# Kernel tuning notes

Hardware: AMD Instinct MI355X
Metric: run time of the kernel (lower is better)

The kernel has to match this reference:

```python
import jax, jax.numpy as jnp
import numpy as np

D_MODEL = 1024
NUM_HEADS = 16
HEAD_DIM = D_MODEL // NUM_HEADS  # 64
SEQ = 2048
BATCH = 4
LN_EPS = 1e-5


def setup_inputs() -> dict:
    key = jax.random.key(0)
    k_in, k_qkv, k_o, k_g = jax.random.split(key, 4)
    inputs = jax.random.normal(k_in, (BATCH, SEQ, D_MODEL), dtype=jnp.float32)
    mask = jnp.zeros((BATCH, 1, SEQ, SEQ), dtype=jnp.float32)  # additive mask
    # Realistic rotary embeddings (RoPE), duplicated-halves layout
    inv_freq = 1.0 / (10000.0 ** (jnp.arange(0, HEAD_DIM, 2, dtype=jnp.float32) / HEAD_DIM))
    pos = jnp.arange(SEQ, dtype=jnp.float32)
    freqs = pos[:, None] * inv_freq[None, :]            # [S, Dh/2]
    emb = jnp.concatenate([freqs, freqs], axis=-1)       # [S, Dh]
    cos = jnp.cos(emb)
    sin = jnp.sin(emb)
    # Parameters
    sd = 1.0 / np.sqrt(D_MODEL)
    w_qkv = jax.random.normal(k_qkv, (D_MODEL, 3 * D_MODEL), dtype=jnp.float32) * sd
    w_o = jax.random.normal(k_o, (D_MODEL, D_MODEL), dtype=jnp.float32) * sd
    ln_gamma = jnp.ones((D_MODEL,), dtype=jnp.float32)
    return {"inputs": inputs, "mask": mask, "cos": cos, "sin": sin,
            "ln_gamma": ln_gamma, "w_qkv": w_qkv, "w_o": w_o}


def _rotate_half(x):
    x1, x2 = jnp.split(x, 2, axis=-1)
    return jnp.concatenate([-x2, x1], axis=-1)


def reference(inputs, mask, cos, sin, ln_gamma, w_qkv, w_o):
    B, S, D = inputs.shape
    # Pre-attention LayerNorm (layer_id != 0), center=False -> no beta
    mu = jnp.mean(inputs, axis=-1, keepdims=True)
    var = jnp.mean(jnp.square(inputs - mu), axis=-1, keepdims=True)
    x = (inputs - mu) / jnp.sqrt(var + LN_EPS) * ln_gamma
    # Fused QKV projection, split into heads: [B, H, S, Dh]
    qkv = (x @ w_qkv).reshape(B, S, 3, NUM_HEADS, HEAD_DIM)
    qkv = jnp.transpose(qkv, (2, 0, 3, 1, 4))
    q, k, v = qkv[0], qkv[1], qkv[2]
    # RoPE
    c = cos.reshape(1, 1, S, HEAD_DIM)
    s = sin.reshape(1, 1, S, HEAD_DIM)
    q = q * c + _rotate_half(q) * s
    k = k * c + _rotate_half(k) * s
    # Scaled dot-product attention with additive mask
    scale = 1.0 / jnp.sqrt(jnp.asarray(HEAD_DIM, dtype=q.dtype))
    logits = jnp.einsum("bhqd,bhkd->bhqk", q, k) * scale + mask
    attn = jax.nn.softmax(logits, axis=-1)
    out = jnp.einsum("bhqk,bhkd->bhqd", attn, v)
    out = jnp.transpose(out, (0, 2, 1, 3)).reshape(B, S, D)
    return out @ w_o
```

## Files before the change

kernel.cpp:

```cpp
#include <hip/hip_runtime.h>
#include <stdint.h>

#define DEV __device__ __forceinline__

typedef __bf16 bf16x8 __attribute__((ext_vector_type(8)));
typedef float f32x4 __attribute__((ext_vector_type(4)));
typedef float f32x16 __attribute__((ext_vector_type(16)));

DEV unsigned short f2bf(float f) {
  union { float f; uint32_t u; } c; c.f = f;
  uint32_t u = c.u;
  u += 0x7FFFu + ((u >> 16) & 1u);
  return (unsigned short)(u >> 16);
}
DEV float bf2f(unsigned short h) {
  union { uint32_t u; float f; } c; c.u = ((uint32_t)h) << 16;
  return c.f;
}
DEV float u2f(uint32_t u) {
  union { uint32_t u; float f; } c; c.u = u;
  return c.f;
}
DEV bf16x8 ld8(const unsigned short* p) {
  uint4 u = *reinterpret_cast<const uint4*>(p);
  return __builtin_bit_cast(bf16x8, u);
}
DEV uint32_t cvtpk(float lo, float hi) {
  uint32_t r;
  asm("v_cvt_pk_bf16_f32 %0, %1, %2" : "=v"(r) : "v"(lo), "v"(hi));
  return r;
}
DEV void permswap(uint32_t& a, uint32_t& b) {
  asm("v_permlane32_swap_b32 %0, %1" : "+v"(a), "+v"(b));
}
DEV float exp2b(float x) { return __builtin_amdgcn_exp2f(x); }
DEV void gload16(const void* g, void* l) {
  __builtin_amdgcn_global_load_lds((const __attribute__((address_space(1))) void*)g,
                                   (__attribute__((address_space(3))) void*)l, 16, 0, 0);
}

template<int K, int N>
__global__ __launch_bounds__(256)
void transpose_cast_kernel(const float* __restrict__ in, unsigned short* __restrict__ out) {
  __shared__ float tile[64][65];
  const int bk = blockIdx.x % (K / 64);
  const int bn = blockIdx.x / (K / 64);
  const int k0 = bk * 64, n0 = bn * 64;
  const int t = threadIdx.x;
#pragma unroll
  for (int i = 0; i < 16; ++i) {
    int idx = t + i * 256;
    int kl = idx >> 6, nl = idx & 63;
    tile[kl][nl] = in[(size_t)(k0 + kl) * N + n0 + nl];
  }
  __syncthreads();
#pragma unroll
  for (int i = 0; i < 16; ++i) {
    int idx = t + i * 256;
    int nl = idx >> 6, kl = idx & 63;
    out[(size_t)(n0 + nl) * K + k0 + kl] = f2bf(tile[kl][nl]);
  }
}

__global__ __launch_bounds__(256)
void ln_kernel(const float* __restrict__ x, const float* __restrict__ gamma,
               unsigned short* __restrict__ y) {
  const int row = blockIdx.x;
  const int t = threadIdx.x;
  const float4 v = reinterpret_cast<const float4*>(x + (size_t)row * 1024)[t];
  float s  = v.x + v.y + v.z + v.w;
  float s2 = v.x * v.x + v.y * v.y + v.z * v.z + v.w * v.w;
#pragma unroll
  for (int off = 1; off < 64; off <<= 1) {
    s  += __shfl_xor(s, off);
    s2 += __shfl_xor(s2, off);
  }
  __shared__ float red[8];
  const int w = t >> 6, lane = t & 63;
  if (lane == 0) { red[w] = s; red[4 + w] = s2; }
  __syncthreads();
  s  = red[0] + red[1] + red[2] + red[3];
  s2 = red[4] + red[5] + red[6] + red[7];
  const float mu = s * (1.0f / 1024.0f);
  const float var = s2 * (1.0f / 1024.0f) - mu * mu;
  const float rstd = rsqrtf(var + 1e-5f);
  const float4 g = reinterpret_cast<const float4*>(gamma)[t];
  ushort4 o;
  o.x = f2bf((v.x - mu) * rstd * g.x);
  o.y = f2bf((v.y - mu) * rstd * g.y);
  o.z = f2bf((v.z - mu) * rstd * g.z);
  o.w = f2bf((v.w - mu) * rstd * g.w);
  reinterpret_cast<ushort4*>(y + (size_t)row * 1024)[t] = o;
}

template<int N_DIM, bool OUT_F32>
__global__ __launch_bounds__(256)
void gemm_bt_kernel(const unsigned short* __restrict__ A,
                    const unsigned short* __restrict__ Bt,
                    void* __restrict__ Cout) {
  constexpr int K = 1024;
  __shared__ unsigned short a_lds[128 * 32];
  __shared__ unsigned short b_lds[128 * 32];
  const int t = threadIdx.x;
  const int w = t >> 6, l = t & 63;
  const int lrow = l & 15, lch = l >> 4;
  const int nbn = N_DIM / 128;
  const int m0 = (blockIdx.x / nbn) * 128;
  const int n0 = (blockIdx.x % nbn) * 128;
  const int wm = (w >> 1) * 64, wn = (w & 1) * 64;

  const int srow = t >> 2;
  const int schk = t & 3;
  const int scol = ((schk ^ (srow & 3)) << 3);
  const unsigned short* aS0 = A  + (size_t)(m0 + srow) * K + scol;
  const unsigned short* aS1 = A  + (size_t)(m0 + 64 + srow) * K + scol;
  const unsigned short* bS0 = Bt + (size_t)(n0 + srow) * K + scol;
  const unsigned short* bS1 = Bt + (size_t)(n0 + 64 + srow) * K + scol;
  unsigned short* aD0 = a_lds + (w * 16) * 32;
  unsigned short* aD1 = a_lds + (64 + w * 16) * 32;
  unsigned short* bD0 = b_lds + (w * 16) * 32;
  unsigned short* bD1 = b_lds + (64 + w * 16) * 32;

  f32x4 acc[4][4] = {};

  for (int k0 = 0; k0 < K; k0 += 32) {
    gload16(aS0 + k0, aD0);
    gload16(aS1 + k0, aD1);
    gload16(bS0 + k0, bD0);
    gload16(bS1 + k0, bD1);
    __syncthreads();
    bf16x8 af[4], bfr[4];
#pragma unroll
    for (int m = 0; m < 4; ++m) {
      int row = wm + m * 16 + lrow;
      af[m] = ld8(a_lds + row * 32 + ((lch ^ (lrow & 3)) << 3));
    }
#pragma unroll
    for (int n = 0; n < 4; ++n) {
      int row = wn + n * 16 + lrow;
      bfr[n] = ld8(b_lds + row * 32 + ((lch ^ (lrow & 3)) << 3));
    }
#pragma unroll
    for (int m = 0; m < 4; ++m)
#pragma unroll
      for (int n = 0; n < 4; ++n)
        acc[m][n] = __builtin_amdgcn_mfma_f32_16x16x32_bf16(af[m], bfr[n], acc[m][n], 0, 0, 0);
    __syncthreads();
  }

#pragma unroll
  for (int m = 0; m < 4; ++m) {
    const int grow0 = m0 + wm + m * 16 + lch * 4;
#pragma unroll
    for (int n = 0; n < 4; ++n) {
      const int gcol = n0 + wn + n * 16 + lrow;
#pragma unroll
      for (int r = 0; r < 4; ++r) {
        if constexpr (OUT_F32)
          ((float*)Cout)[(size_t)(grow0 + r) * N_DIM + gcol] = acc[m][n][r];
        else
          ((unsigned short*)Cout)[(size_t)(grow0 + r) * N_DIM + gcol] = f2bf(acc[m][n][r]);
      }
    }
  }
}

__global__ __launch_bounds__(256)
void rope_split_kernel(const unsigned short* __restrict__ qkv,
                       const float* __restrict__ cosb,
                       const float* __restrict__ sinb,
                       unsigned short* __restrict__ Qo,
                       unsigned short* __restrict__ Ko,
                       unsigned short* __restrict__ Vo) {
  const int bid = blockIdx.x;
  const int sb = bid & 31, h = (bid >> 5) & 15, b = bid >> 9;
  const int s0 = sb * 64;
  const int t = threadIdx.x;
  __shared__ unsigned short qt[64][72], kt[64][72], vt[64][72];

  const int sl = t >> 2, c0 = (t & 3) * 16;
  {
    const size_t base = (size_t)(b * 2048 + s0 + sl) * 3072 + h * 64 + c0;
    uint4 q1 = *(const uint4*)(qkv + base);
    uint4 q2 = *(const uint4*)(qkv + base + 8);
    uint4 k1 = *(const uint4*)(qkv + base + 1024);
    uint4 k2 = *(const uint4*)(qkv + base + 1032);
    uint4 v1 = *(const uint4*)(qkv + base + 2048);
    uint4 v2 = *(const uint4*)(qkv + base + 2056);
    *(uint4*)&qt[sl][c0] = q1; *(uint4*)&qt[sl][c0 + 8] = q2;
    *(uint4*)&kt[sl][c0] = k1; *(uint4*)&kt[sl][c0 + 8] = k2;
    *(uint4*)&vt[sl][c0] = v1; *(uint4*)&vt[sl][c0 + 8] = v2;
  }
  __syncthreads();
  {
    const int sg = s0 + sl;
    alignas(16) unsigned short qo16[16], ko16[16];
#pragma unroll
    for (int j = 0; j < 16; ++j) {
      const int d = c0 + j;
      const float cv = cosb[sg * 64 + d], sv = sinb[sg * 64 + d];
      const float qv = bf2f(qt[sl][d]), qp = bf2f(qt[sl][d ^ 32]);
      const float kv = bf2f(kt[sl][d]), kp = bf2f(kt[sl][d ^ 32]);
      const float rq = qv * cv + ((d < 32) ? -qp : qp) * sv;
      const float rk = kv * cv + ((d < 32) ? -kp : kp) * sv;
      qo16[j] = f2bf(rq * 0.180336880f);
      ko16[j] = f2bf(rk);
    }
    const size_t ob = ((size_t)(b * 16 + h) * 2048 + sg) * 64 + c0;
    *(uint4*)(Qo + ob) = *(uint4*)qo16; *(uint4*)(Qo + ob + 8) = *(uint4*)(qo16 + 8);
    *(uint4*)(Ko + ob) = *(uint4*)ko16; *(uint4*)(Ko + ob + 8) = *(uint4*)(ko16 + 8);
  }
  {
    const int dh = t >> 2, sc0 = (t & 3) * 16;
    alignas(16) unsigned short vo16[16];
#pragma unroll
    for (int j = 0; j < 16; ++j) vo16[j] = vt[sc0 + j][dh];
    const size_t ob = ((size_t)(b * 16 + h) * 64 + dh) * 2048 + s0 + sc0;
    *(uint4*)(Vo + ob) = *(uint4*)vo16; *(uint4*)(Vo + ob + 8) = *(uint4*)(vo16 + 8);
  }
}

__global__ __launch_bounds__(256)
void mask_prep_kernel(const float* __restrict__ mask, unsigned short* __restrict__ mrs,
                      unsigned char* __restrict__ flg) {
  const int bid = blockIdx.x;
  const int kvt = bid & 31, qc = (bid >> 5) & 31, b = bid >> 10;
  const int t = threadIdx.x;
  __shared__ float tile[64][72];
  __shared__ int nzf;
  if (t == 0) nzf = 0;
  uint32_t orbits = 0;
  {
    const int r = t >> 2, c0 = (t & 3) * 16;
    const float* src = mask + (size_t)b * (2048ull * 2048) + (size_t)(qc * 64 + r) * 2048 + kvt * 64 + c0;
#pragma unroll
    for (int i = 0; i < 4; ++i) {
      const float4 v = *(const float4*)(src + i * 4);
      *(float4*)&tile[r][c0 + i * 4] = v;
      orbits |= __float_as_uint(v.x) | __float_as_uint(v.y) |
                __float_as_uint(v.z) | __float_as_uint(v.w);
    }
  }
  __syncthreads();
  if (orbits != 0u) nzf = 1;
  __syncthreads();
  if (nzf) {
    const int cid = t >> 5;
    const int n = cid >> 2, jj = (cid >> 1) & 1, hi = cid & 1;
    const int qq0 = (t & 31) * 2;
    const int cb = n * 32 + jj * 16 + hi * 4;
    unsigned short* dst = mrs + (((size_t)(b * 32 + kvt) * 8 + cid) * 2048 + qc * 64) * 8;
#pragma unroll
    for (int qo = 0; qo < 2; ++qo) {
      const int q = qq0 + qo;
      alignas(16) unsigned short o8[8];
#pragma unroll
      for (int v = 0; v < 8; ++v) {
        const int col = cb + (v >> 2) * 8 + (v & 3);
        o8[v] = f2bf(tile[q][col] * 1.44269504f);
      }
      *(uint4*)(dst + (size_t)q * 8) = *(uint4*)o8;
    }
  }
  if (t == 0) flg[(size_t)(b * 32 + kvt) * 32 + qc] = (unsigned char)nzf;
}

__global__ __launch_bounds__(256)
void attn_kernel(const unsigned short* __restrict__ Q,
                 const unsigned short* __restrict__ Kg,
                 const unsigned short* __restrict__ Vt,
                 const unsigned short* __restrict__ mrs,
                 const unsigned char* __restrict__ flg,
                 unsigned short* __restrict__ O) {
  const int t = threadIdx.x, w = t >> 6, l = t & 63;
  const int lq = l & 31, hi = l >> 5;
  const int bid = blockIdx.x;
  const int x = bid & 7, y = bid >> 3;
  const int bh = x * 8 + (y & 7), qb = y >> 3;
  const int b = bh >> 4, h = bh & 15;
  const int q0 = qb * 128 + w * 32;

  const unsigned short* Qb = Q  + (size_t)bh * (2048 * 64);
  const unsigned short* Kb = Kg + (size_t)bh * (2048 * 64);
  const unsigned short* Vb = Vt + (size_t)bh * (64 * 2048);
  const unsigned short* ml = mrs + (size_t)b * 4194304 + (size_t)hi * 16384 + (size_t)(q0 + lq) * 8;
  const unsigned char* fb = flg + (size_t)(b * 32) * 32 + qb * 2;

  __shared__ unsigned short k_lds[2][64 * 64];
  __shared__ unsigned short v_lds[2][64 * 64];

  bf16x8 qf[4];
  {
    const unsigned short* qp = Qb + (size_t)(q0 + lq) * 64 + hi * 8;
#pragma unroll
    for (int c = 0; c < 4; ++c) qf[c] = ld8(qp + c * 16);
  }
  bf16x8 ones;
  {
    const uint4 ou = { 0x3F803F80u, 0x3F803F80u, 0x3F803F80u, 0x3F803F80u };
    ones = __builtin_bit_cast(bf16x8, ou);
  }

  const int srow = t >> 2, sl0 = (t & 3) * 2, sl1 = sl0 + 1;
  const unsigned short* ks = Kb + (size_t)srow * 64 + sl0 * 8;
  const unsigned short* vs = Vb + (size_t)srow * 2048 + sl0 * 8;
  const int wd0 = srow * 64 + ((sl0 ^ (srow & 7)) << 3);
  const int wd1 = srow * 64 + ((sl1 ^ (srow & 7)) << 3);

  uint4 ka0 = *(const uint4*)ks;
  uint4 ka1 = *(const uint4*)(ks + 8);
  uint4 va0 = *(const uint4*)vs;
  uint4 va1 = *(const uint4*)(vs + 8);
  *(uint4*)(k_lds[0] + wd0) = ka0;
  *(uint4*)(k_lds[0] + wd1) = ka1;
  *(uint4*)(v_lds[0] + wd0) = va0;
  *(uint4*)(v_lds[0] + wd1) = va1;

  f32x16 ot0 = {}, ot1 = {};
  f32x16 st_sum = {};
  int cur = 0;
  const int lsw = lq & 7;

  uint4 mA[4], mB[4];

  auto do_tile = [&](int kv0, uint4 (&mcur)[4], uint4 (&mnext)[4],
                     bool hm, bool hmn) {
    __syncthreads();
    const bool more = (kv0 + 64) < 2048;
    if (more) {
      ka0 = *(const uint4*)(ks + (size_t)(kv0 + 64) * 64);
      ka1 = *(const uint4*)(ks + (size_t)(kv0 + 64) * 64 + 8);
      va0 = *(const uint4*)(vs + kv0 + 64);
      va1 = *(const uint4*)(vs + kv0 + 64 + 8);
      if (hmn) {
        const unsigned short* mp = ml + (size_t)(kv0 + 64) * 2048;
#pragma unroll
        for (int c2 = 0; c2 < 4; ++c2) mnext[c2] = *(const uint4*)(mp + c2 * 32768);
      }
    }

    f32x16 st0 = {}, st1 = {};
    if (hm) {
#pragma unroll
      for (int jj = 0; jj < 2; ++jj) {
        const uint4 u0 = mcur[jj];
        const uint4 u1 = mcur[2 + jj];
#pragma unroll
        for (int wv = 0; wv < 4; ++wv) {
          const uint32_t w0 = ((const uint32_t*)&u0)[wv];
          const uint32_t w1 = ((const uint32_t*)&u1)[wv];
          st0[jj * 8 + wv * 2]     = u2f(w0 << 16);
          st0[jj * 8 + wv * 2 + 1] = u2f(w0 & 0xffff0000u);
          st1[jj * 8 + wv * 2]     = u2f(w1 << 16);
          st1[jj * 8 + wv * 2 + 1] = u2f(w1 & 0xffff0000u);
        }
      }
    }

    const unsigned short* kb = k_lds[cur];
    __builtin_amdgcn_s_setprio(1);
#pragma unroll
    for (int c = 0; c < 4; ++c) {
      const int so = (((2 * c + hi) ^ lsw) << 3);
      const bf16x8 kf0 = ld8(kb + lq * 64 + so);
      const bf16x8 kf1 = ld8(kb + (32 + lq) * 64 + so);
      st0 = __builtin_amdgcn_mfma_f32_32x32x16_bf16(kf0, qf[c], st0, 0, 0, 0);
      st1 = __builtin_amdgcn_mfma_f32_32x32x16_bf16(kf1, qf[c], st1, 0, 0, 0);
    }
    __builtin_amdgcn_s_setprio(0);

#pragma unroll
    for (int r = 0; r < 16; ++r) {
      st0[r] = exp2b(st0[r]);
      st1[r] = exp2b(st1[r]);
    }

    bf16x8 pa[4];
#pragma unroll
    for (int c = 0; c < 4; ++c) {
      const int e8 = (c & 1) * 8;
      uint32_t A01, B01, A23, B23;
      if (c < 2) {
        A01 = cvtpk(st0[e8 + 0], st0[e8 + 1]);
        B01 = cvtpk(st0[e8 + 4], st0[e8 + 5]);
        A23 = cvtpk(st0[e8 + 2], st0[e8 + 3]);
        B23 = cvtpk(st0[e8 + 6], st0[e8 + 7]);
      } else {
        A01 = cvtpk(st1[e8 + 0], st1[e8 + 1]);
        B01 = cvtpk(st1[e8 + 4], st1[e8 + 5]);
        A23 = cvtpk(st1[e8 + 2], st1[e8 + 3]);
        B23 = cvtpk(st1[e8 + 6], st1[e8 + 7]);
      }
      permswap(A01, B01);
      permswap(A23, B23);
      const uint4 pw = { A01, A23, B01, B23 };
      pa[c] = __builtin_bit_cast(bf16x8, pw);
    }

    if (more) {
      unsigned short* kn = k_lds[cur ^ 1];
      unsigned short* vn = v_lds[cur ^ 1];
      *(uint4*)(kn + wd0) = ka0;
      *(uint4*)(kn + wd1) = ka1;
      *(uint4*)(vn + wd0) = va0;
      *(uint4*)(vn + wd1) = va1;
    }

    const unsigned short* vb = v_lds[cur];
    __builtin_amdgcn_s_setprio(1);
#pragma unroll
    for (int c = 0; c < 4; ++c) {
      const int so = (((2 * c + hi) ^ lsw) << 3);
      const bf16x8 vf0 = ld8(vb + lq * 64 + so);
      const bf16x8 vf1 = ld8(vb + (32 + lq) * 64 + so);
      ot0 = __builtin_amdgcn_mfma_f32_32x32x16_bf16(vf0, pa[c], ot0, 0, 0, 0);
      ot1 = __builtin_amdgcn_mfma_f32_32x32x16_bf16(vf1, pa[c], ot1, 0, 0, 0);
      st_sum = __builtin_amdgcn_mfma_f32_32x32x16_bf16(ones, pa[c], st_sum, 0, 0, 0);
    }
    __builtin_amdgcn_s_setprio(0);
    cur ^= 1;
  };

  unsigned int bm = 0;
  for (int kvt = 0; kvt < 32; ++kvt) bm |= fb[kvt * 32] | fb[kvt * 32 + 1];

  if (bm == 0) {
    for (int kv0 = 0; kv0 < 2048; kv0 += 128) {
      do_tile(kv0, mA, mB, false, false);
      do_tile(kv0 + 64, mB, mA, false, false);
    }
  } else {
    bool hmA = (fb[0] | fb[1]) != 0;
    if (hmA) {
#pragma unroll
      for (int c2 = 0; c2 < 4; ++c2) mA[c2] = *(const uint4*)(ml + c2 * 32768);
    }
    bool hmB = false;
    for (int kv0 = 0; kv0 < 2048; kv0 += 128) {
      const int tB = (kv0 >> 6) + 1;
      hmB = (kv0 + 64 < 2048) && ((fb[tB * 32] | fb[tB * 32 + 1]) != 0);
      do_tile(kv0, mA, mB, hmA, hmB);
      const int tA = tB + 1;
      hmA = (kv0 + 128 < 2048) && ((fb[tA * 32] | fb[tA * 32 + 1]) != 0);
      do_tile(kv0 + 64, mB, mA, hmB, hmA);
    }
  }

  const float inv = 1.0f / st_sum[0];
  unsigned short* ob = O + ((size_t)(b * 2048 + q0 + lq) * 16 + h) * 64 + hi * 4;
#pragma unroll
  for (int td = 0; td < 2; ++td) {
#pragma unroll
    for (int rr = 0; rr < 4; ++rr) {
      ushort4 ov;
      if (td == 0) {
        ov.x = f2bf(ot0[rr * 4 + 0] * inv);
        ov.y = f2bf(ot0[rr * 4 + 1] * inv);
        ov.z = f2bf(ot0[rr * 4 + 2] * inv);
        ov.w = f2bf(ot0[rr * 4 + 3] * inv);
      } else {
        ov.x = f2bf(ot1[rr * 4 + 0] * inv);
        ov.y = f2bf(ot1[rr * 4 + 1] * inv);
        ov.z = f2bf(ot1[rr * 4 + 2] * inv);
        ov.w = f2bf(ot1[rr * 4 + 3] * inv);
      }
      *(ushort4*)(ob + td * 32 + rr * 8) = ov;
    }
  }
}

extern "C" void kernel_launch(void* const* d_in, const int* in_sizes, int n_in,
                              void* d_out, int out_size, void* d_ws, size_t ws_size,
                              hipStream_t stream) {
  (void)in_sizes; (void)n_in; (void)out_size; (void)ws_size;
  const float* x     = (const float*)d_in[0];
  const float* mask  = (const float*)d_in[1];
  const float* cosb  = (const float*)d_in[2];
  const float* sinb  = (const float*)d_in[3];
  const float* gamma = (const float*)d_in[4];
  const float* w_qkv = (const float*)d_in[5];
  const float* w_o   = (const float*)d_in[6];

  char* ws = (char*)d_ws;
  unsigned short* x_bf   = (unsigned short*)(ws);
  unsigned short* wqkvT  = (unsigned short*)(ws + 16777216);
  unsigned short* woT    = (unsigned short*)(ws + 23068672);
  unsigned short* qkv_bf = (unsigned short*)(ws + 25165824);
  unsigned short* q_r    = (unsigned short*)(ws + 75497472);
  unsigned short* k_r    = (unsigned short*)(ws + 92274688);
  unsigned short* v_t    = (unsigned short*)(ws + 109051904);
  unsigned short* attn   = (unsigned short*)(ws + 125829120);
  unsigned short* mask_rs = qkv_bf;
  unsigned char*  flags   = (unsigned char*)(ws + 25165824 + 33554432);

  transpose_cast_kernel<1024, 3072><<<dim3(16 * 48), dim3(256), 0, stream>>>(w_qkv, wqkvT);
  transpose_cast_kernel<1024, 1024><<<dim3(16 * 16), dim3(256), 0, stream>>>(w_o, woT);
  ln_kernel<<<dim3(8192), dim3(256), 0, stream>>>(x, gamma, x_bf);
  gemm_bt_kernel<3072, false><<<dim3(64 * 24), dim3(256), 0, stream>>>(x_bf, wqkvT, (void*)qkv_bf);
  rope_split_kernel<<<dim3(4 * 16 * 32), dim3(256), 0, stream>>>(qkv_bf, cosb, sinb, q_r, k_r, v_t);
  mask_prep_kernel<<<dim3(4096), dim3(256), 0, stream>>>(mask, mask_rs, flags);
  attn_kernel<<<dim3(1024), dim3(256), 0, stream>>>(q_r, k_r, v_t, mask_rs, flags, attn);
  gemm_bt_kernel<1024, true><<<dim3(64 * 8), dim3(256), 0, stream>>>(attn, woT, d_out);
}
```

Measured before the change: 237.4 us.

## Pre-swizzle K/V into MFMA fragment layout and load directly to registers

```diff
diff --git a/kernel.cpp b/kernel.cpp
--- a/kernel.cpp
+++ b/kernel.cpp
@@ -170,8 +170,8 @@
                        const float* __restrict__ cosb,
                        const float* __restrict__ sinb,
                        unsigned short* __restrict__ Qo,
-                       unsigned short* __restrict__ Ko,
-                       unsigned short* __restrict__ Vo) {
+                       unsigned short* __restrict__ Kf,
+                       unsigned short* __restrict__ Vf) {
   const int bid = blockIdx.x;
   const int sb = bid & 31, h = (bid >> 5) & 15, b = bid >> 9;
   const int s0 = sb * 64;
@@ -192,6 +192,7 @@
     *(uint4*)&vt[sl][c0] = v1; *(uint4*)&vt[sl][c0 + 8] = v2;
   }
   __syncthreads();
+  const size_t fbase = (size_t)(b * 16 + h) * 131072;
   {
     const int sg = s0 + sl;
     alignas(16) unsigned short qo16[16], ko16[16];
@@ -208,15 +209,18 @@
     }
     const size_t ob = ((size_t)(b * 16 + h) * 2048 + sg) * 64 + c0;
     *(uint4*)(Qo + ob) = *(uint4*)qo16; *(uint4*)(Qo + ob + 8) = *(uint4*)(qo16 + 8);
-    *(uint4*)(Ko + ob) = *(uint4*)ko16; *(uint4*)(Ko + ob + 8) = *(uint4*)(ko16 + 8);
+    unsigned short* kd = Kf + fbase + ((size_t)((sb * 2 + (sl >> 5)) * 4 + (t & 3))) * 512;
+    *(uint4*)(kd + (sl & 31) * 8)        = *(uint4*)ko16;
+    *(uint4*)(kd + (32 + (sl & 31)) * 8) = *(uint4*)(ko16 + 8);
   }
   {
     const int dh = t >> 2, sc0 = (t & 3) * 16;
     alignas(16) unsigned short vo16[16];
 #pragma unroll
     for (int j = 0; j < 16; ++j) vo16[j] = vt[sc0 + j][dh];
-    const size_t ob = ((size_t)(b * 16 + h) * 64 + dh) * 2048 + s0 + sc0;
-    *(uint4*)(Vo + ob) = *(uint4*)vo16; *(uint4*)(Vo + ob + 8) = *(uint4*)(vo16 + 8);
+    unsigned short* vd = Vf + fbase + ((size_t)((sb * 2 + (dh >> 5)) * 4 + (t & 3))) * 512;
+    *(uint4*)(vd + (dh & 31) * 8)        = *(uint4*)vo16;
+    *(uint4*)(vd + (32 + (dh & 31)) * 8) = *(uint4*)(vo16 + 8);
   }
 }
 
@@ -267,8 +271,8 @@
 
 __global__ __launch_bounds__(256)
 void attn_kernel(const unsigned short* __restrict__ Q,
-                 const unsigned short* __restrict__ Kg,
-                 const unsigned short* __restrict__ Vt,
+                 const unsigned short* __restrict__ Kf,
+                 const unsigned short* __restrict__ Vf,
                  const unsigned short* __restrict__ mrs,
                  const unsigned char* __restrict__ flg,
                  unsigned short* __restrict__ O) {
@@ -280,15 +284,12 @@
   const int b = bh >> 4, h = bh & 15;
   const int q0 = qb * 128 + w * 32;
 
-  const unsigned short* Qb = Q  + (size_t)bh * (2048 * 64);
-  const unsigned short* Kb = Kg + (size_t)bh * (2048 * 64);
-  const unsigned short* Vb = Vt + (size_t)bh * (64 * 2048);
+  const unsigned short* Qb  = Q  + (size_t)bh * (2048 * 64);
+  const unsigned short* Kfb = Kf + (size_t)bh * 131072;
+  const unsigned short* Vfb = Vf + (size_t)bh * 131072;
   const unsigned short* ml = mrs + (size_t)b * 4194304 + (size_t)hi * 16384 + (size_t)(q0 + lq) * 8;
   const unsigned char* fb = flg + (size_t)(b * 32) * 32 + qb * 2;
 
-  __shared__ unsigned short k_lds[2][64 * 64];
-  __shared__ unsigned short v_lds[2][64 * 64];
-
   bf16x8 qf[4];
   {
     const unsigned short* qp = Qb + (size_t)(q0 + lq) * 64 + hi * 8;
@@ -301,42 +302,26 @@
     ones = __builtin_bit_cast(bf16x8, ou);
   }
 
-  const int srow = t >> 2, sl0 = (t & 3) * 2, sl1 = sl0 + 1;
-  const unsigned short* ks = Kb + (size_t)srow * 64 + sl0 * 8;
-  const unsigned short* vs = Vb + (size_t)srow * 2048 + sl0 * 8;
-  const int wd0 = srow * 64 + ((sl0 ^ (srow & 7)) << 3);
-  const int wd1 = srow * 64 + ((sl1 ^ (srow & 7)) << 3);
-
-  uint4 ka0 = *(const uint4*)ks;
-  uint4 ka1 = *(const uint4*)(ks + 8);
-  uint4 va0 = *(const uint4*)vs;
-  uint4 va1 = *(const uint4*)(vs + 8);
-  *(uint4*)(k_lds[0] + wd0) = ka0;
-  *(uint4*)(k_lds[0] + wd1) = ka1;
-  *(uint4*)(v_lds[0] + wd0) = va0;
-  *(uint4*)(v_lds[0] + wd1) = va1;
-
   f32x16 ot0 = {}, ot1 = {};
   f32x16 st_sum = {};
-  int cur = 0;
-  const int lsw = lq & 7;
 
   uint4 mA[4], mB[4];
 
-  auto do_tile = [&](int kv0, uint4 (&mcur)[4], uint4 (&mnext)[4],
+  auto do_tile = [&](int kvt, uint4 (&mcur)[4], uint4 (&mnext)[4],
                      bool hm, bool hmn) {
-    __syncthreads();
-    const bool more = (kv0 + 64) < 2048;
-    if (more) {
-      ka0 = *(const uint4*)(ks + (size_t)(kv0 + 64) * 64);
-      ka1 = *(const uint4*)(ks + (size_t)(kv0 + 64) * 64 + 8);
-      va0 = *(const uint4*)(vs + kv0 + 64);
-      va1 = *(const uint4*)(vs + kv0 + 64 + 8);
-      if (hmn) {
-        const unsigned short* mp = ml + (size_t)(kv0 + 64) * 2048;
-#pragma unroll
-        for (int c2 = 0; c2 < 4; ++c2) mnext[c2] = *(const uint4*)(mp + c2 * 32768);
-      }
+    const unsigned short* kp = Kfb + (size_t)kvt * 4096 + l * 8;
+    const unsigned short* vp = Vfb + (size_t)kvt * 4096 + l * 8;
+    uint4 kr[8], vr[8];
+#pragma unroll
+    for (int i = 0; i < 8; ++i) kr[i] = *(const uint4*)(kp + i * 512);
+#pragma unroll
+    for (int i = 0; i < 8; ++i) vr[i] = *(const uint4*)(vp + i * 512);
+
+    const bool more = (kvt + 1) < 32;
+    if (more && hmn) {
+      const unsigned short* mp = ml + (size_t)(kvt + 1) * 131072;
+#pragma unroll
+      for (int c2 = 0; c2 < 4; ++c2) mnext[c2] = *(const uint4*)(mp + c2 * 32768);
     }
 
     f32x16 st0 = {}, st1 = {};
@@ -357,15 +342,11 @@
       }
     }
 
-    const unsigned short* kb = k_lds[cur];
     __builtin_amdgcn_s_setprio(1);
 #pragma unroll
     for (int c = 0; c < 4; ++c) {
-      const int so = (((2 * c + hi) ^ lsw) << 3);
-      const bf16x8 kf0 = ld8(kb + lq * 64 + so);
-      const bf16x8 kf1 = ld8(kb + (32 + lq) * 64 + so);
-      st0 = __builtin_amdgcn_mfma_f32_32x32x16_bf16(kf0, qf[c], st0, 0, 0, 0);
-      st1 = __builtin_amdgcn_mfma_f32_32x32x16_bf16(kf1, qf[c], st1, 0, 0, 0);
+      st0 = __builtin_amdgcn_mfma_f32_32x32x16_bf16(__builtin_bit_cast(bf16x8, kr[c]),     qf[c], st0, 0, 0, 0);
+      st1 = __builtin_amdgcn_mfma_f32_32x32x16_bf16(__builtin_bit_cast(bf16x8, kr[4 + c]), qf[c], st1, 0, 0, 0);
     }
     __builtin_amdgcn_s_setprio(0);
 
@@ -397,37 +378,23 @@
       pa[c] = __builtin_bit_cast(bf16x8, pw);
     }
 
-    if (more) {
-      unsigned short* kn = k_lds[cur ^ 1];
-      unsigned short* vn = v_lds[cur ^ 1];
-      *(uint4*)(kn + wd0) = ka0;
-      *(uint4*)(kn + wd1) = ka1;
-      *(uint4*)(vn + wd0) = va0;
-      *(uint4*)(vn + wd1) = va1;
-    }
-
-    const unsigned short* vb = v_lds[cur];
     __builtin_amdgcn_s_setprio(1);
 #pragma unroll
     for (int c = 0; c < 4; ++c) {
-      const int so = (((2 * c + hi) ^ lsw) << 3);
-      const bf16x8 vf0 = ld8(vb + lq * 64 + so);
-      const bf16x8 vf1 = ld8(vb + (32 + lq) * 64 + so);
-      ot0 = __builtin_amdgcn_mfma_f32_32x32x16_bf16(vf0, pa[c], ot0, 0, 0, 0);
-      ot1 = __builtin_amdgcn_mfma_f32_32x32x16_bf16(vf1, pa[c], ot1, 0, 0, 0);
+      ot0 = __builtin_amdgcn_mfma_f32_32x32x16_bf16(__builtin_bit_cast(bf16x8, vr[c]),     pa[c], ot0, 0, 0, 0);
+      ot1 = __builtin_amdgcn_mfma_f32_32x32x16_bf16(__builtin_bit_cast(bf16x8, vr[4 + c]), pa[c], ot1, 0, 0, 0);
       st_sum = __builtin_amdgcn_mfma_f32_32x32x16_bf16(ones, pa[c], st_sum, 0, 0, 0);
     }
     __builtin_amdgcn_s_setprio(0);
-    cur ^= 1;
   };
 
   unsigned int bm = 0;
   for (int kvt = 0; kvt < 32; ++kvt) bm |= fb[kvt * 32] | fb[kvt * 32 + 1];
 
   if (bm == 0) {
-    for (int kv0 = 0; kv0 < 2048; kv0 += 128) {
-      do_tile(kv0, mA, mB, false, false);
-      do_tile(kv0 + 64, mB, mA, false, false);
+    for (int kvt = 0; kvt < 32; kvt += 2) {
+      do_tile(kvt, mA, mB, false, false);
+      do_tile(kvt + 1, mB, mA, false, false);
     }
   } else {
     bool hmA = (fb[0] | fb[1]) != 0;
@@ -436,13 +403,12 @@
       for (int c2 = 0; c2 < 4; ++c2) mA[c2] = *(const uint4*)(ml + c2 * 32768);
     }
     bool hmB = false;
-    for (int kv0 = 0; kv0 < 2048; kv0 += 128) {
-      const int tB = (kv0 >> 6) + 1;
-      hmB = (kv0 + 64 < 2048) && ((fb[tB * 32] | fb[tB * 32 + 1]) != 0);
-      do_tile(kv0, mA, mB, hmA, hmB);
-      const int tA = tB + 1;
-      hmA = (kv0 + 128 < 2048) && ((fb[tA * 32] | fb[tA * 32 + 1]) != 0);
-      do_tile(kv0 + 64, mB, mA, hmB, hmA);
+    for (int kvt = 0; kvt < 32; kvt += 2) {
+      hmB = (kvt + 1 < 32) && ((fb[(kvt + 1) * 32] | fb[(kvt + 1) * 32 + 1]) != 0);
+      do_tile(kvt, mA, mB, hmA, hmB);
+      const bool hmA2 = (kvt + 2 < 32) && ((fb[(kvt + 2) * 32] | fb[(kvt + 2) * 32 + 1]) != 0);
+      do_tile(kvt + 1, mB, mA, hmB, hmA2);
+      hmA = hmA2;
     }
   }
 
@@ -487,8 +453,8 @@
   unsigned short* woT    = (unsigned short*)(ws + 23068672);
   unsigned short* qkv_bf = (unsigned short*)(ws + 25165824);
   unsigned short* q_r    = (unsigned short*)(ws + 75497472);
-  unsigned short* k_r    = (unsigned short*)(ws + 92274688);
-  unsigned short* v_t    = (unsigned short*)(ws + 109051904);
+  unsigned short* k_f    = (unsigned short*)(ws + 92274688);
+  unsigned short* v_f    = (unsigned short*)(ws + 109051904);
   unsigned short* attn   = (unsigned short*)(ws + 125829120);
   unsigned short* mask_rs = qkv_bf;
   unsigned char*  flags   = (unsigned char*)(ws + 25165824 + 33554432);
@@ -497,8 +463,8 @@
   transpose_cast_kernel<1024, 1024><<<dim3(16 * 16), dim3(256), 0, stream>>>(w_o, woT);
   ln_kernel<<<dim3(8192), dim3(256), 0, stream>>>(x, gamma, x_bf);
   gemm_bt_kernel<3072, false><<<dim3(64 * 24), dim3(256), 0, stream>>>(x_bf, wqkvT, (void*)qkv_bf);
-  rope_split_kernel<<<dim3(4 * 16 * 32), dim3(256), 0, stream>>>(qkv_bf, cosb, sinb, q_r, k_r, v_t);
+  rope_split_kernel<<<dim3(4 * 16 * 32), dim3(256), 0, stream>>>(qkv_bf, cosb, sinb, q_r, k_f, v_f);
   mask_prep_kernel<<<dim3(4096), dim3(256), 0, stream>>>(mask, mask_rs, flags);
-  attn_kernel<<<dim3(1024), dim3(256), 0, stream>>>(q_r, k_r, v_t, mask_rs, flags, attn);
+  attn_kernel<<<dim3(1024), dim3(256), 0, stream>>>(q_r, k_f, v_f, mask_rs, flags, attn);
   gemm_bt_kernel<1024, true><<<dim3(64 * 8), dim3(256), 0, stream>>>(attn, woT, d_out);
 }
```

Result: slower. 260.8 us (+9.9%).
